# Performance work log

Measured on AMD Instinct MI355X. Metric: run time of the kernel, lower is better.

The kernel has to match this reference:

```python
import jax, jax.numpy as jnp
import numpy as np

B, S, F = 256, 512, 26
H, M, C = 512, 256, 20  # rnn_hidden, mlp_hidden, num_classes


def setup_inputs() -> dict:
    key = jax.random.key(0)
    ks = jax.random.split(key, 9)
    s_ih = 1.0 / np.sqrt(H)
    return {
        "x": jax.random.normal(ks[0], (B, S, F), dtype=jnp.float32),
        "w_ih": jax.random.uniform(ks[1], (4 * H, F), jnp.float32, -s_ih, s_ih),
        "w_hh": jax.random.uniform(ks[2], (4 * H, H), jnp.float32, -s_ih, s_ih),
        "b_ih": jax.random.uniform(ks[3], (4 * H,), jnp.float32, -s_ih, s_ih),
        "b_hh": jax.random.uniform(ks[4], (4 * H,), jnp.float32, -s_ih, s_ih),
        "w1": jax.random.uniform(ks[5], (M, H), jnp.float32, -s_ih, s_ih),
        "b1": jax.random.uniform(ks[6], (M,), jnp.float32, -s_ih, s_ih),
        "w2": jax.random.uniform(ks[7], (C, M), jnp.float32, -1.0 / np.sqrt(M), 1.0 / np.sqrt(M)),
        "b2": jax.random.uniform(ks[8], (C,), jnp.float32, -1.0 / np.sqrt(M), 1.0 / np.sqrt(M)),
    }


def reference(x, w_ih, w_hh, b_ih, b_hh, w1, b1, w2, b2):
    b, s, _ = x.shape
    h0 = jnp.zeros((b, H), x.dtype)
    c0 = jnp.zeros((b, H), x.dtype)
    bias = b_ih + b_hh

    def step(carry, xt):
        h, c = carry
        # original stores hx.data -> state carried into next step is detached
        h = jax.lax.stop_gradient(h)
        c = jax.lax.stop_gradient(c)
        z = xt @ w_ih.T + h @ w_hh.T + bias  # [b, 4H]
        i, f, g, o = jnp.split(z, 4, axis=-1)  # PyTorch gate order i,f,g,o
        c2 = jax.nn.sigmoid(f) * c + jax.nn.sigmoid(i) * jnp.tanh(g)
        h2 = jax.nn.sigmoid(o) * jnp.tanh(c2)
        return (h2, c2), h2

    _, hs = jax.lax.scan(step, (h0, c0), jnp.transpose(x, (1, 0, 2)))  # hs: [s, b, H]
    hs = jnp.transpose(hs, (1, 0, 2))  # [b, s, H]
    hidden = jax.nn.relu(jnp.einsum("bsh,mh->bsm", hs, w1) + b1)
    logits = jnp.einsum("bsm,cm->bsc", hidden, w2) + b2
    return jax.nn.log_softmax(logits, axis=-1)
```

## Files before the change

kernel.cpp:

```cpp
#include <hip/hip_runtime.h>

#define S_LEN 512
#define HID   512
#define FEAT  26
#define NCLS  20
#define DRING 16

typedef short bf16x8 __attribute__((ext_vector_type(8)));
typedef float f32x4  __attribute__((ext_vector_type(4)));

__device__ __forceinline__ unsigned short f2bf(float f) {
    unsigned u = __builtin_bit_cast(unsigned, f);
    unsigned r = (u + 0x7FFFu + ((u >> 16) & 1u)) >> 16;
    return (unsigned short)r;
}
__device__ __forceinline__ float sigm(float x) { return 1.f / (1.f + __expf(-x)); }
__device__ __forceinline__ float tanh_f(float x) {
    float xc = fminf(fmaxf(x, -15.f), 15.f);
    float t = __expf(-2.f * xc);
    return (1.f - t) / (1.f + t);
}

__device__ __forceinline__ void load4_coherent(const unsigned short* p,
                                               uint4& a0, uint4& a1, uint4& a2, uint4& a3) {
    asm volatile(
        "global_load_dwordx4 %0, %4, off sc0 sc1\n\t"
        "global_load_dwordx4 %1, %5, off sc0 sc1\n\t"
        "global_load_dwordx4 %2, %6, off sc0 sc1\n\t"
        "global_load_dwordx4 %3, %7, off sc0 sc1\n\t"
        "s_waitcnt vmcnt(0)"
        : "=&v"(a0), "=&v"(a1), "=&v"(a2), "=&v"(a3)
        : "v"(p), "v"(p + 8), "v"(p + 16), "v"(p + 24)
        : "memory");
}
__device__ __forceinline__ void store_coherent(unsigned short* p, unsigned d) {
    asm volatile(
        "global_store_dword %0, %1, off sc0 sc1\n\t"
        "s_waitcnt vmcnt(0)"
        :: "v"(p), "v"(d) : "memory");
}
__device__ __forceinline__ void store_coherent_x2(unsigned short* p, unsigned long long d) {
    asm volatile(
        "global_store_dwordx2 %0, %1, off sc0 sc1\n\t"
        "s_waitcnt vmcnt(0)"
        :: "v"(p), "v"(d) : "memory");
}
__device__ __forceinline__ void store_u32_nowait(unsigned* p, unsigned d) {
    asm volatile("global_store_dword %0, %1, off sc0 sc1" :: "v"(p), "v"(d) : "memory");
}
__device__ __forceinline__ unsigned load_u32_coherent(const unsigned* p) {
    unsigned v;
    asm volatile("global_load_dword %0, %1, off sc0 sc1\n\ts_waitcnt vmcnt(0)"
                 : "=v"(v) : "v"(p) : "memory");
    return v;
}
__device__ __forceinline__ void store_u32_sys_wait(unsigned* p, unsigned d) {
    asm volatile("global_store_dword %0, %1, off sc0 sc1\n\ts_waitcnt vmcnt(0)"
                 :: "v"(p), "v"(d) : "memory");
}

__device__ __forceinline__ void load4_l2(const unsigned short* p,
                                         uint4& a0, uint4& a1, uint4& a2, uint4& a3) {
    asm volatile(
        "global_load_dwordx4 %0, %4, off sc0\n\t"
        "global_load_dwordx4 %1, %5, off sc0\n\t"
        "global_load_dwordx4 %2, %6, off sc0\n\t"
        "global_load_dwordx4 %3, %7, off sc0\n\t"
        "s_waitcnt vmcnt(0)"
        : "=&v"(a0), "=&v"(a1), "=&v"(a2), "=&v"(a3)
        : "v"(p), "v"(p + 8), "v"(p + 16), "v"(p + 24)
        : "memory");
}
__device__ __forceinline__ void store_l2_x2(unsigned short* p, unsigned long long d) {
    asm volatile(
        "global_store_dwordx2 %0, %1, off sc0\n\t"
        "s_waitcnt vmcnt(0)"
        :: "v"(p), "v"(d) : "memory");
}
__device__ __forceinline__ void store_u32_nowait_l2(unsigned* p, unsigned d) {
    asm volatile("global_store_dword %0, %1, off sc0" :: "v"(p), "v"(d) : "memory");
}
__device__ __forceinline__ unsigned load_u32_l2(const unsigned* p) {
    unsigned v;
    asm volatile("global_load_dword %0, %1, off sc0\n\ts_waitcnt vmcnt(0)"
                 : "=v"(v) : "v"(p) : "memory");
    return v;
}

__global__ void prep_kernel(const float* __restrict__ w1, const float* __restrict__ w2,
                            unsigned short* __restrict__ w1b, unsigned short* __restrict__ w2b,
                            unsigned* __restrict__ syncw, int nclear) {
    int i = blockIdx.x * 256 + threadIdx.x;
    if (i < nclear) syncw[i] = 0u;
    if (i < 256 * 512) w1b[i] = f2bf(w1[i]);
    if (i < NCLS * 256) w2b[i] = f2bf(w2[i]);
}

__global__ __launch_bounds__(256, 1) void lstm_big_kernel(
    const float* __restrict__ x,
    const float* __restrict__ w_ih,
    const float* __restrict__ w_hh,
    const float* __restrict__ b_ih,
    const float* __restrict__ b_hh,
    const unsigned short* __restrict__ w1b,
    const float* __restrict__ b1,
    const unsigned short* __restrict__ w2b,
    const float* __restrict__ b2,
    float* __restrict__ out,
    unsigned short* __restrict__ hs,
    unsigned* __restrict__ flags)
{
    const int tid  = threadIdx.x;
    const int wave = tid >> 6;
    const int lane = tid & 63;
    const int quad = lane >> 4;
    const int l16  = lane & 15;

    const int  bx      = blockIdx.x;
    const int  xasm    = bx & 7;
    const int  kslt    = bx >> 3;
    const bool is_lstm = (kslt < 16);
    const int  ksub    = is_lstm ? kslt : (kslt - 16);
    const int  clust   = xasm * 2 + (ksub >> 3);
    const int  sub     = ksub & 7;

    __shared__ __align__(16) unsigned short At[16 * 552];
    __shared__ __align__(16) unsigned short hid[16 * 264];
    __shared__ float lg[16 * 24];
    __shared__ unsigned rdy;
    __shared__ unsigned fastf;
    if (tid == 0) rdy = 0u;

    {
        unsigned xcc;
        asm volatile("s_getreg_b32 %0, hwreg(HW_REG_XCC_ID)" : "=s"(xcc));
        if (tid == 0) {
            unsigned* slot = flags + (clust * 8 + sub) * 16 + (is_lstm ? 8 : 9);
            store_u32_sys_wait(slot, (xcc & 0xFu) + 1u);
        }
        if (wave == 0) {
            const unsigned* ps = flags + (clust * 8 + (lane & 7)) * 16 + ((lane & 8) ? 9 : 8);
            unsigned myx = 1u;
            for (;;) {
                unsigned v = 1u;
                if (lane < 16) v = load_u32_coherent(ps);
                if (__ballot(v != 0u) == ~0ull) { myx = v; break; }
                __builtin_amdgcn_s_sleep(2);
            }
            unsigned ref = __shfl(myx, 0);
            bool eq = (lane >= 16) || (myx == ref);
            if (tid == 0) fastf = (__ballot(eq) == ~0ull) ? 1u : 0u;
        }
    }
    __syncthreads();
    const bool fast = (fastf != 0u);

    if (is_lstm) {
        const int wic = sub;
        const int B0  = clust * 16;
        const int U0  = wic * 64;

        bf16x8 bB[4][17];
#pragma unroll
        for (int g = 0; g < 4; ++g) {
            const int row = g * 512 + U0 + wave * 16 + l16;
            const float* wrow = w_hh + (size_t)row * HID;
#pragma unroll
            for (int kk = 0; kk < 16; ++kk) {
                const float* p = wrow + kk * 32 + quad * 8;
                bf16x8 v;
#pragma unroll
                for (int j = 0; j < 8; ++j) v[j] = (short)f2bf(p[j]);
                bB[g][kk] = v;
            }
            const float* irow = w_ih + (size_t)row * FEAT;
            bf16x8 v;
#pragma unroll
            for (int j = 0; j < 8; ++j) {
                int ftr = quad * 8 + j;
                v[j] = (ftr < FEAT) ? (short)f2bf(irow[ftr]) : (short)0;
            }
            bB[g][16] = v;
        }

        float bias[4][4];
#pragma unroll
        for (int g = 0; g < 4; ++g)
#pragma unroll
            for (int r = 0; r < 4; ++r) {
                int rr = g * 512 + U0 + wave * 16 + quad * 4 + r;
                bias[g][r] = b_ih[rr] + b_hh[rr];
            }
        float cst[4] = {0.f, 0.f, 0.f, 0.f};

        const int sm = tid >> 4;
        const int sc = tid & 15;
        unsigned short* hsc = hs + (size_t)clust * S_LEN * 16 * HID;
        unsigned* myflag = flags + (clust * 8 + wic) * 16;
        const unsigned* peer = flags + (clust * 8 + (lane & 7)) * 16;

        for (int t = 0; t < S_LEN; ++t) {
            {
                unsigned pk = 0u;
                if (sc <= 12) {
                    float2 xv = *(const float2*)(x + ((size_t)(B0 + sm) * S_LEN + t) * FEAT + sc * 2);
                    pk = (unsigned)f2bf(xv.x) | ((unsigned)f2bf(xv.y) << 16);
                }
                *(unsigned*)(At + sm * 552 + 512 + sc * 2) = pk;
            }
            if (t > 0) {
                const unsigned tt = (unsigned)t;
                for (;;) {
                    unsigned v = ~0u;
                    if (lane < 8) v = fast ? load_u32_l2(peer) : load_u32_coherent(peer);
                    if (__ballot(v >= tt) == ~0ull) break;
                    if (!fast) __builtin_amdgcn_s_sleep(1);
                }
                const unsigned short* src =
                    hsc + ((size_t)(t - 1) * 16 + sm) * HID + sc * 32;
                unsigned short* dst = At + sm * 552 + sc * 32;
                uint4 a0, a1, a2, a3;
                if (fast) load4_l2(src, a0, a1, a2, a3);
                else      load4_coherent(src, a0, a1, a2, a3);
                *(uint4*)(dst)      = a0;
                *(uint4*)(dst + 8)  = a1;
                *(uint4*)(dst + 16) = a2;
                *(uint4*)(dst + 24) = a3;
            }
            __syncthreads();

            f32x4 acc[4];
#pragma unroll
            for (int g = 0; g < 4; ++g) acc[g] = (f32x4){0.f, 0.f, 0.f, 0.f};
            const unsigned short* arow = At + l16 * 552 + quad * 8;
            if (t > 0) {
#pragma unroll
                for (int kk = 0; kk < 17; ++kk) {
                    bf16x8 h = __builtin_bit_cast(bf16x8, *(const uint4*)(arow + kk * 32));
#pragma unroll
                    for (int g = 0; g < 4; ++g)
                        acc[g] = __builtin_amdgcn_mfma_f32_16x16x32_bf16(bB[g][kk], h, acc[g], 0, 0, 0);
                }
            } else {
                bf16x8 h = __builtin_bit_cast(bf16x8, *(const uint4*)(arow + 16 * 32));
#pragma unroll
                for (int g = 0; g < 4; ++g)
                    acc[g] = __builtin_amdgcn_mfma_f32_16x16x32_bf16(bB[g][16], h, acc[g], 0, 0, 0);
            }

            {
                unsigned short hv[4];
#pragma unroll
                for (int r = 0; r < 4; ++r) {
                    float zi = acc[0][r] + bias[0][r];
                    float zf = acc[1][r] + bias[1][r];
                    float zg = acc[2][r] + bias[2][r];
                    float zo = acc[3][r] + bias[3][r];
                    float cn = sigm(zf) * cst[r] + sigm(zi) * tanh_f(zg);
                    cst[r] = cn;
                    hv[r] = f2bf(sigm(zo) * tanh_f(cn));
                }
                unsigned long long d = (unsigned long long)hv[0]
                                     | ((unsigned long long)hv[1] << 16)
                                     | ((unsigned long long)hv[2] << 32)
                                     | ((unsigned long long)hv[3] << 48);
                unsigned short* hp = hsc + ((size_t)t * 16 + l16) * HID
                                   + U0 + wave * 16 + quad * 4;
                if (fast) store_l2_x2(hp, d);
                else      store_coherent_x2(hp, d);
            }
            __syncthreads();
            if (tid == 0) {
                if (fast) store_u32_nowait_l2(myflag, (unsigned)(t + 1));
                else      store_u32_nowait(myflag, (unsigned)(t + 1));
            }
        }
    } else {
        const int mc  = clust;
        const int m   = sub;
        const int B0  = mc * 16;
        const unsigned* peer = flags + (mc * 8 + (lane & 7)) * 16;
        const unsigned short* hsc = hs + (size_t)mc * S_LEN * 16 * HID;
        const int sm = tid >> 4;
        const int sc = tid & 15;

        for (int t = m; t < S_LEN; t += 8) {
            if (wave == 0) {
                for (;;) {
                    unsigned v = fast ? load_u32_l2(peer) : load_u32_coherent(peer);
                    if (__ballot(v >= (unsigned)(t + 1)) == ~0ull) break;
                    __builtin_amdgcn_s_sleep(8);
                }
                if (lane == 0)
                    __hip_atomic_store(&rdy, (unsigned)(t + 1), __ATOMIC_RELAXED,
                                       __HIP_MEMORY_SCOPE_WORKGROUP);
            } else {
                while (__hip_atomic_load(&rdy, __ATOMIC_RELAXED,
                                         __HIP_MEMORY_SCOPE_WORKGROUP) < (unsigned)(t + 1))
                    __builtin_amdgcn_s_sleep(8);
            }
            {
                const unsigned short* src = hsc + ((size_t)t * 16 + sm) * HID + sc * 32;
                unsigned short* dst = At + sm * 552 + sc * 32;
                uint4 a0, a1, a2, a3;
                if (fast) load4_l2(src, a0, a1, a2, a3);
                else      load4_coherent(src, a0, a1, a2, a3);
                *(uint4*)(dst)      = a0;
                *(uint4*)(dst + 8)  = a1;
                *(uint4*)(dst + 16) = a2;
                *(uint4*)(dst + 24) = a3;
            }
            __syncthreads();

            f32x4 a1[4];
#pragma unroll
            for (int nt = 0; nt < 4; ++nt) a1[nt] = (f32x4){0.f, 0.f, 0.f, 0.f};
#pragma unroll
            for (int kk = 0; kk < 16; ++kk) {
                bf16x8 a = __builtin_bit_cast(
                    bf16x8, *(const uint4*)(At + l16 * 552 + kk * 32 + quad * 8));
#pragma unroll
                for (int nt = 0; nt < 4; ++nt) {
                    int n = wave * 64 + nt * 16 + l16;
                    bf16x8 b = __builtin_bit_cast(
                        bf16x8, *(const uint4*)(w1b + (size_t)n * 512 + kk * 32 + quad * 8));
                    a1[nt] = __builtin_amdgcn_mfma_f32_16x16x32_bf16(a, b, a1[nt], 0, 0, 0);
                }
            }
#pragma unroll
            for (int nt = 0; nt < 4; ++nt) {
                int n = wave * 64 + nt * 16 + l16;
                float bv = b1[n];
#pragma unroll
                for (int r = 0; r < 4; ++r)
                    hid[(quad * 4 + r) * 264 + n] = f2bf(fmaxf(a1[nt][r] + bv, 0.f));
            }
            __syncthreads();
            if (wave == 0) {
                f32x4 a2[2];
                a2[0] = (f32x4){0.f, 0.f, 0.f, 0.f};
                a2[1] = (f32x4){0.f, 0.f, 0.f, 0.f};
#pragma unroll
                for (int kk = 0; kk < 8; ++kk) {
                    bf16x8 a = __builtin_bit_cast(
                        bf16x8, *(const uint4*)(hid + l16 * 264 + kk * 32 + quad * 8));
#pragma unroll
                    for (int nt = 0; nt < 2; ++nt) {
                        int n = nt * 16 + l16;
                        bf16x8 b;
                        if (n < NCLS) {
                            b = __builtin_bit_cast(
                                bf16x8, *(const uint4*)(w2b + (size_t)n * 256 + kk * 32 + quad * 8));
                        } else {
                            uint4 z; z.x = z.y = z.z = z.w = 0u;
                            b = __builtin_bit_cast(bf16x8, z);
                        }
                        a2[nt] = __builtin_amdgcn_mfma_f32_16x16x32_bf16(a, b, a2[nt], 0, 0, 0);
                    }
                }
#pragma unroll
                for (int nt = 0; nt < 2; ++nt) {
                    int n = nt * 16 + l16;
                    if (n < NCLS) {
                        float bv = b2[n];
#pragma unroll
                        for (int r = 0; r < 4; ++r)
                            lg[(quad * 4 + r) * 24 + n] = a2[nt][r] + bv;
                    }
                }
            }
            __syncthreads();
            if (tid < 16) {
                float v[NCLS];
                float mx = -3.4e38f;
#pragma unroll
                for (int c = 0; c < NCLS; ++c) { v[c] = lg[tid * 24 + c]; mx = fmaxf(mx, v[c]); }
                float s = 0.f;
#pragma unroll
                for (int c = 0; c < NCLS; ++c) s += __expf(v[c] - mx);
                float lse = mx + __logf(s);
                float* orow = out + ((size_t)(B0 + tid) * S_LEN + t) * NCLS;
#pragma unroll
                for (int c = 0; c < NCLS; ++c) orow[c] = v[c] - lse;
            }
            __syncthreads();
        }
    }
}

__global__ __launch_bounds__(256, 2) void lstm_fused_kernel(
    const float* __restrict__ x, const float* __restrict__ w_ih,
    const float* __restrict__ w_hh, const float* __restrict__ b_ih,
    const float* __restrict__ b_hh, const unsigned short* __restrict__ w1b,
    const float* __restrict__ b1, const unsigned short* __restrict__ w2b,
    const float* __restrict__ b2, float* __restrict__ out,
    unsigned short* __restrict__ hb, unsigned* __restrict__ flags,
    unsigned* __restrict__ done)
{
    const int tid  = threadIdx.x;
    const int wave = tid >> 6;
    const int lane = tid & 63;
    const int quad = lane >> 4;
    const int l16  = lane & 15;
    const int wg   = blockIdx.x;

    __shared__ __align__(16) unsigned short At[16 * 552];
    __shared__ float zb[16 * 132];
    __shared__ __align__(16) unsigned short hid[16 * 264];
    __shared__ float lg[16 * 24];
    __shared__ unsigned rdy;
    if (tid == 0) rdy = 0u;
    __syncthreads();

    if (wg < 256) {
        const int clust = (wg & 7) * 2 + (wg >= 128 ? 1 : 0);
        const int wic   = (wg >> 3) & 15;
        const int B0    = clust * 16;
        const int U0    = wic * 32;

        bf16x8 bB[2][17];
#pragma unroll
        for (int tl = 0; tl < 2; ++tl) {
            const int row = wave * 512 + U0 + tl * 16 + l16;
            const float* wrow = w_hh + (size_t)row * HID;
#pragma unroll
            for (int kk = 0; kk < 16; ++kk) {
                const float* p = wrow + kk * 32 + quad * 8;
                bf16x8 v;
#pragma unroll
                for (int j = 0; j < 8; ++j) v[j] = (short)f2bf(p[j]);
                bB[tl][kk] = v;
            }
            const float* irow = w_ih + (size_t)row * FEAT;
            bf16x8 v;
#pragma unroll
            for (int j = 0; j < 8; ++j) {
                int ftr = quad * 8 + j;
                v[j] = (ftr < FEAT) ? (short)f2bf(irow[ftr]) : (short)0;
            }
            bB[tl][16] = v;
        }

        const int gb = tid >> 4;
        const int gu = tid & 15;
        float bias[2][4];
#pragma unroll
        for (int uu = 0; uu < 2; ++uu)
#pragma unroll
            for (int g = 0; g < 4; ++g) {
                int r = g * 512 + U0 + 2 * gu + uu;
                bias[uu][g] = b_ih[r] + b_hh[r];
            }
        float cst[2] = {0.f, 0.f};

        const int sm = tid >> 4;
        const int sc = tid & 15;
        unsigned short* hbc = hb + (size_t)clust * DRING * 16 * HID;
        unsigned* myflag = flags + (clust * 16 + wic) * 16;
        const unsigned* peer = flags + (clust * 16 + (lane & 15)) * 16;

        for (int t = 0; t < S_LEN; ++t) {
            {
                unsigned pk = 0u;
                if (sc <= 12) {
                    float2 xv = *(const float2*)(x + ((size_t)(B0 + sm) * S_LEN + t) * FEAT + sc * 2);
                    pk = (unsigned)f2bf(xv.x) | ((unsigned)f2bf(xv.y) << 16);
                }
                *(unsigned*)(At + sm * 552 + 512 + sc * 2) = pk;
            }
            if (t > 0) {
                if (wave == 0) {
                    if (t >= DRING && lane == 0) {
                        const unsigned* dn = done + (clust * 8 + (t & 7)) * 16;
                        while (load_u32_coherent(dn) < (unsigned)(t - (DRING - 1)))
                            __builtin_amdgcn_s_sleep(8);
                    }
                    for (;;) {
                        unsigned v = load_u32_coherent(peer);
                        if (__ballot(v >= (unsigned)t) == ~0ull) break;
                        __builtin_amdgcn_s_sleep(1);
                    }
                    if (lane == 0)
                        __hip_atomic_store(&rdy, (unsigned)t, __ATOMIC_RELAXED,
                                           __HIP_MEMORY_SCOPE_WORKGROUP);
                } else {
                    while (__hip_atomic_load(&rdy, __ATOMIC_RELAXED,
                                             __HIP_MEMORY_SCOPE_WORKGROUP) < (unsigned)t)
                        __builtin_amdgcn_s_sleep(1);
                }
                const unsigned short* src =
                    hbc + ((t - 1) & (DRING - 1)) * 16 * HID + sm * HID + sc * 32;
                unsigned short* dst = At + sm * 552 + sc * 32;
                uint4 a0, a1, a2, a3;
                load4_coherent(src, a0, a1, a2, a3);
                *(uint4*)(dst)      = a0;
                *(uint4*)(dst + 8)  = a1;
                *(uint4*)(dst + 16) = a2;
                *(uint4*)(dst + 24) = a3;
            }
            __syncthreads();

            f32x4 acc0 = {0.f, 0.f, 0.f, 0.f};
            f32x4 acc1 = {0.f, 0.f, 0.f, 0.f};
            const unsigned short* arow = At + l16 * 552 + quad * 8;
            if (t > 0) {
#pragma unroll
                for (int kk = 0; kk < 17; ++kk) {
                    bf16x8 a = __builtin_bit_cast(bf16x8, *(const uint4*)(arow + kk * 32));
                    acc0 = __builtin_amdgcn_mfma_f32_16x16x32_bf16(a, bB[0][kk], acc0, 0, 0, 0);
                    acc1 = __builtin_amdgcn_mfma_f32_16x16x32_bf16(a, bB[1][kk], acc1, 0, 0, 0);
                }
            } else {
                bf16x8 a = __builtin_bit_cast(bf16x8, *(const uint4*)(arow + 16 * 32));
                acc0 = __builtin_amdgcn_mfma_f32_16x16x32_bf16(a, bB[0][16], acc0, 0, 0, 0);
                acc1 = __builtin_amdgcn_mfma_f32_16x16x32_bf16(a, bB[1][16], acc1, 0, 0, 0);
            }
#pragma unroll
            for (int r = 0; r < 4; ++r) {
                zb[(quad * 4 + r) * 132 + wave * 32 + l16]      = acc0[r];
                zb[(quad * 4 + r) * 132 + wave * 32 + 16 + l16] = acc1[r];
            }
            __syncthreads();

            {
                const float* zrow = zb + gb * 132;
                unsigned short hv2[2];
#pragma unroll
                for (int uu = 0; uu < 2; ++uu) {
                    int u = 2 * gu + uu;
                    float zi = zrow[u]      + bias[uu][0];
                    float zf = zrow[32 + u] + bias[uu][1];
                    float zg = zrow[64 + u] + bias[uu][2];
                    float zo = zrow[96 + u] + bias[uu][3];
                    float cn = sigm(zf) * cst[uu] + sigm(zi) * tanh_f(zg);
                    cst[uu] = cn;
                    hv2[uu] = f2bf(sigm(zo) * tanh_f(cn));
                }
                unsigned short* hp =
                    hbc + (t & (DRING - 1)) * 16 * HID + gb * HID + U0 + 2 * gu;
                store_coherent(hp, (unsigned)hv2[0] | ((unsigned)hv2[1] << 16));
            }
            __syncthreads();
            if (tid == 0) store_u32_nowait(myflag, (unsigned)(t + 1));
        }
    } else {
        const int mwg  = wg - 256;
        const int mc   = mwg >> 3;
        const int m    = mwg & 7;
        const int B0   = mc * 16;
        unsigned* mydone = done + (mc * 8 + m) * 16;
        const unsigned* peer = flags + (mc * 16 + (lane & 15)) * 16;
        const unsigned short* hbc = hb + (size_t)mc * DRING * 16 * HID;
        const int sm = tid >> 4;
        const int sc = tid & 15;

        for (int t = m; t < S_LEN; t += 8) {
            if (wave == 0) {
                for (;;) {
                    unsigned v = load_u32_coherent(peer);
                    if (__ballot(v >= (unsigned)(t + 1)) == ~0ull) break;
                    __builtin_amdgcn_s_sleep(8);
                }
                if (lane == 0)
                    __hip_atomic_store(&rdy, (unsigned)(t + 1), __ATOMIC_RELAXED,
                                       __HIP_MEMORY_SCOPE_WORKGROUP);
            } else {
                while (__hip_atomic_load(&rdy, __ATOMIC_RELAXED,
                                         __HIP_MEMORY_SCOPE_WORKGROUP) < (unsigned)(t + 1))
                    __builtin_amdgcn_s_sleep(8);
            }
            {
                const unsigned short* src =
                    hbc + (t & (DRING - 1)) * 16 * HID + sm * HID + sc * 32;
                unsigned short* dst = At + sm * 552 + sc * 32;
                uint4 a0, a1, a2, a3;
                load4_coherent(src, a0, a1, a2, a3);
                *(uint4*)(dst)      = a0;
                *(uint4*)(dst + 8)  = a1;
                *(uint4*)(dst + 16) = a2;
                *(uint4*)(dst + 24) = a3;
            }
            __syncthreads();
            if (tid == 0) store_u32_nowait(mydone, (unsigned)(t + 1));

            f32x4 a1[4];
#pragma unroll
            for (int nt = 0; nt < 4; ++nt) a1[nt] = (f32x4){0.f, 0.f, 0.f, 0.f};
#pragma unroll
            for (int kk = 0; kk < 16; ++kk) {
                bf16x8 a = __builtin_bit_cast(
                    bf16x8, *(const uint4*)(At + l16 * 552 + kk * 32 + quad * 8));
#pragma unroll
                for (int nt = 0; nt < 4; ++nt) {
                    int n = wave * 64 + nt * 16 + l16;
                    bf16x8 b = __builtin_bit_cast(
                        bf16x8, *(const uint4*)(w1b + (size_t)n * 512 + kk * 32 + quad * 8));
                    a1[nt] = __builtin_amdgcn_mfma_f32_16x16x32_bf16(a, b, a1[nt], 0, 0, 0);
                }
            }
#pragma unroll
            for (int nt = 0; nt < 4; ++nt) {
                int n = wave * 64 + nt * 16 + l16;
                float bv = b1[n];
#pragma unroll
                for (int r = 0; r < 4; ++r)
                    hid[(quad * 4 + r) * 264 + n] = f2bf(fmaxf(a1[nt][r] + bv, 0.f));
            }
            __syncthreads();
            if (wave == 0) {
                f32x4 a2[2];
                a2[0] = (f32x4){0.f, 0.f, 0.f, 0.f};
                a2[1] = (f32x4){0.f, 0.f, 0.f, 0.f};
#pragma unroll
                for (int kk = 0; kk < 8; ++kk) {
                    bf16x8 a = __builtin_bit_cast(
                        bf16x8, *(const uint4*)(hid + l16 * 264 + kk * 32 + quad * 8));
#pragma unroll
                    for (int nt = 0; nt < 2; ++nt) {
                        int n = nt * 16 + l16;
                        bf16x8 b;
                        if (n < NCLS) {
                            b = __builtin_bit_cast(
                                bf16x8, *(const uint4*)(w2b + (size_t)n * 256 + kk * 32 + quad * 8));
                        } else {
                            uint4 z; z.x = z.y = z.z = z.w = 0u;
                            b = __builtin_bit_cast(bf16x8, z);
                        }
                        a2[nt] = __builtin_amdgcn_mfma_f32_16x16x32_bf16(a, b, a2[nt], 0, 0, 0);
                    }
                }
#pragma unroll
                for (int nt = 0; nt < 2; ++nt) {
                    int n = nt * 16 + l16;
                    if (n < NCLS) {
                        float bv = b2[n];
#pragma unroll
                        for (int r = 0; r < 4; ++r)
                            lg[(quad * 4 + r) * 24 + n] = a2[nt][r] + bv;
                    }
                }
            }
            __syncthreads();
            if (tid < 16) {
                float v[NCLS];
                float mx = -3.4e38f;
#pragma unroll
                for (int c = 0; c < NCLS; ++c) { v[c] = lg[tid * 24 + c]; mx = fmaxf(mx, v[c]); }
                float s = 0.f;
#pragma unroll
                for (int c = 0; c < NCLS; ++c) s += __expf(v[c] - mx);
                float lse = mx + __logf(s);
                float* orow = out + ((size_t)(B0 + tid) * S_LEN + t) * NCLS;
#pragma unroll
                for (int c = 0; c < NCLS; ++c) orow[c] = v[c] - lse;
            }
            __syncthreads();
        }
    }
}

extern "C" void kernel_launch(void* const* d_in, const int* in_sizes, int n_in,
                              void* d_out, int out_size, void* d_ws, size_t ws_size,
                              hipStream_t stream) {
    const float* x    = (const float*)d_in[0];
    const float* w_ih = (const float*)d_in[1];
    const float* w_hh = (const float*)d_in[2];
    const float* b_ih = (const float*)d_in[3];
    const float* b_hh = (const float*)d_in[4];
    const float* w1   = (const float*)d_in[5];
    const float* b1   = (const float*)d_in[6];
    const float* w2   = (const float*)d_in[7];
    const float* b2   = (const float*)d_in[8];
    char* ws = (char*)d_ws;

    const size_t HS_BYTES = (size_t)16 * S_LEN * 16 * HID * 2;
    const size_t NEED_BIG = HS_BYTES + 8192 + 262144 + 10240;

    if (ws_size >= NEED_BIG) {
        unsigned short* hsb   = (unsigned short*)ws;
        unsigned*       flags = (unsigned*)(ws + HS_BYTES);
        unsigned short* w1b   = (unsigned short*)(ws + HS_BYTES + 8192);
        unsigned short* w2b   = (unsigned short*)(ws + HS_BYTES + 8192 + 262144);
        prep_kernel<<<512, 256, 0, stream>>>(w1, w2, w1b, w2b, flags, 2048);
        lstm_big_kernel<<<256, 256, 0, stream>>>(x, w_ih, w_hh, b_ih, b_hh,
                                                 w1b, b1, w2b, b2,
                                                 (float*)d_out, hsb, flags);
    } else {
        unsigned short* hb    = (unsigned short*)ws;
        unsigned*       flags = (unsigned*)(ws + 4194304);
        unsigned*       done  = (unsigned*)(ws + 4194304 + 16384);
        unsigned short* w1b   = (unsigned short*)(ws + 4194304 + 16384 + 8192);
        unsigned short* w2b   = (unsigned short*)(ws + 4194304 + 16384 + 8192 + 262144);
        prep_kernel<<<512, 256, 0, stream>>>(w1, w2, w1b, w2b, flags, 6144);
        lstm_fused_kernel<<<384, 256, 0, stream>>>(x, w_ih, w_hh, b_ih, b_hh,
                                                   w1b, b1, w2b, b2,
                                                   (float*)d_out, hb, flags, done);
    }
}
```

Measured before the change: 2.091 ms.

## Load h and x directly into MFMA registers, skipping LDS staging and barrier

Each wave now loads its MFMA B-operand fragments of the previous hidden state straight from global/L2 into registers, and builds the x fragment in registers, instead of staging through an LDS tile with a __syncthreads. Loads are issued without waiting and split with vmcnt(8), so the first half of the MFMAs overlaps the second half of the loads. This removes the LDS round trip and the block barrier from the serial recurrence critical path. In exchange each wave redundantly fetches the full h row set, which raises L2 traffic and register pressure.

```diff
diff --git a/kernel.cpp b/kernel.cpp
--- a/kernel.cpp
+++ b/kernel.cpp
@@ -58,6 +58,17 @@
     asm volatile("global_store_dword %0, %1, off sc0 sc1\n\ts_waitcnt vmcnt(0)"
                  :: "v"(p), "v"(d) : "memory");
 }
+__device__ __forceinline__ void load4_nw_sys(const unsigned short* p,
+                                             uint4& a0, uint4& a1, uint4& a2, uint4& a3) {
+    asm volatile(
+        "global_load_dwordx4 %0, %4, off sc0 sc1\n\t"
+        "global_load_dwordx4 %1, %5, off sc0 sc1\n\t"
+        "global_load_dwordx4 %2, %6, off sc0 sc1\n\t"
+        "global_load_dwordx4 %3, %7, off sc0 sc1"
+        : "=&v"(a0), "=&v"(a1), "=&v"(a2), "=&v"(a3)
+        : "v"(p), "v"(p + 32), "v"(p + 64), "v"(p + 96)
+        : "memory");
+}
 
 __device__ __forceinline__ void load4_l2(const unsigned short* p,
                                          uint4& a0, uint4& a1, uint4& a2, uint4& a3) {
@@ -85,6 +96,17 @@
     asm volatile("global_load_dword %0, %1, off sc0\n\ts_waitcnt vmcnt(0)"
                  : "=v"(v) : "v"(p) : "memory");
     return v;
+}
+__device__ __forceinline__ void load4_nw_l2(const unsigned short* p,
+                                            uint4& a0, uint4& a1, uint4& a2, uint4& a3) {
+    asm volatile(
+        "global_load_dwordx4 %0, %4, off sc0\n\t"
+        "global_load_dwordx4 %1, %5, off sc0\n\t"
+        "global_load_dwordx4 %2, %6, off sc0\n\t"
+        "global_load_dwordx4 %3, %7, off sc0"
+        : "=&v"(a0), "=&v"(a1), "=&v"(a2), "=&v"(a3)
+        : "v"(p), "v"(p + 32), "v"(p + 64), "v"(p + 96)
+        : "memory");
 }
 
 __global__ void prep_kernel(const float* __restrict__ w1, const float* __restrict__ w2,
@@ -193,21 +215,36 @@
             }
         float cst[4] = {0.f, 0.f, 0.f, 0.f};
 
-        const int sm = tid >> 4;
-        const int sc = tid & 15;
         unsigned short* hsc = hs + (size_t)clust * S_LEN * 16 * HID;
         unsigned* myflag = flags + (clust * 8 + wic) * 16;
         const unsigned* peer = flags + (clust * 8 + (lane & 7)) * 16;
+        const float* xrow = x + (size_t)(B0 + l16) * S_LEN * FEAT;
 
         for (int t = 0; t < S_LEN; ++t) {
+            bf16x8 xf;
             {
-                unsigned pk = 0u;
-                if (sc <= 12) {
-                    float2 xv = *(const float2*)(x + ((size_t)(B0 + sm) * S_LEN + t) * FEAT + sc * 2);
-                    pk = (unsigned)f2bf(xv.x) | ((unsigned)f2bf(xv.y) << 16);
-                }
-                *(unsigned*)(At + sm * 552 + 512 + sc * 2) = pk;
-            }
+                const float* xp = xrow + (size_t)t * FEAT + quad * 8;
+                float xv[8];
+                if (quad < 3) {
+                    float2 p0 = *(const float2*)(xp);
+                    float2 p1 = *(const float2*)(xp + 2);
+                    float2 p2 = *(const float2*)(xp + 4);
+                    float2 p3 = *(const float2*)(xp + 6);
+                    xv[0] = p0.x; xv[1] = p0.y; xv[2] = p1.x; xv[3] = p1.y;
+                    xv[4] = p2.x; xv[5] = p2.y; xv[6] = p3.x; xv[7] = p3.y;
+                } else {
+                    float2 p0 = *(const float2*)(xp);
+                    xv[0] = p0.x; xv[1] = p0.y;
+                    xv[2] = xv[3] = xv[4] = xv[5] = xv[6] = xv[7] = 0.f;
+                }
+#pragma unroll
+                for (int j = 0; j < 8; ++j) xf[j] = (short)f2bf(xv[j]);
+            }
+
+            f32x4 acc[4];
+#pragma unroll
+            for (int g = 0; g < 4; ++g) acc[g] = (f32x4){0.f, 0.f, 0.f, 0.f};
+
             if (t > 0) {
                 const unsigned tt = (unsigned)t;
                 for (;;) {
@@ -216,36 +253,52 @@
                     if (__ballot(v >= tt) == ~0ull) break;
                     if (!fast) __builtin_amdgcn_s_sleep(1);
                 }
-                const unsigned short* src =
-                    hsc + ((size_t)(t - 1) * 16 + sm) * HID + sc * 32;
-                unsigned short* dst = At + sm * 552 + sc * 32;
-                uint4 a0, a1, a2, a3;
-                if (fast) load4_l2(src, a0, a1, a2, a3);
-                else      load4_coherent(src, a0, a1, a2, a3);
-                *(uint4*)(dst)      = a0;
-                *(uint4*)(dst + 8)  = a1;
-                *(uint4*)(dst + 16) = a2;
-                *(uint4*)(dst + 24) = a3;
-            }
-            __syncthreads();
-
-            f32x4 acc[4];
-#pragma unroll
-            for (int g = 0; g < 4; ++g) acc[g] = (f32x4){0.f, 0.f, 0.f, 0.f};
-            const unsigned short* arow = At + l16 * 552 + quad * 8;
-            if (t > 0) {
-#pragma unroll
-                for (int kk = 0; kk < 17; ++kk) {
-                    bf16x8 h = __builtin_bit_cast(bf16x8, *(const uint4*)(arow + kk * 32));
-#pragma unroll
-                    for (int g = 0; g < 4; ++g)
-                        acc[g] = __builtin_amdgcn_mfma_f32_16x16x32_bf16(bB[g][kk], h, acc[g], 0, 0, 0);
+                const unsigned short* hrow =
+                    hsc + ((size_t)(t - 1) * 16 + l16) * HID + quad * 8;
+                uint4 hb0, hb1, hb2, hb3, hb4, hb5, hb6, hb7;
+                uint4 hb8, hb9, hb10, hb11, hb12, hb13, hb14, hb15;
+                if (fast) {
+                    load4_nw_l2(hrow,        hb0,  hb1,  hb2,  hb3);
+                    load4_nw_l2(hrow + 128,  hb4,  hb5,  hb6,  hb7);
+                    load4_nw_l2(hrow + 256,  hb8,  hb9,  hb10, hb11);
+                    load4_nw_l2(hrow + 384,  hb12, hb13, hb14, hb15);
+                } else {
+                    load4_nw_sys(hrow,       hb0,  hb1,  hb2,  hb3);
+                    load4_nw_sys(hrow + 128, hb4,  hb5,  hb6,  hb7);
+                    load4_nw_sys(hrow + 256, hb8,  hb9,  hb10, hb11);
+                    load4_nw_sys(hrow + 384, hb12, hb13, hb14, hb15);
+                }
+                asm volatile("s_waitcnt vmcnt(8)" ::: "memory");
+                __builtin_amdgcn_sched_barrier(0);
+#pragma unroll
+                for (int g = 0; g < 4; ++g) {
+                    acc[g] = __builtin_amdgcn_mfma_f32_16x16x32_bf16(bB[g][0], __builtin_bit_cast(bf16x8, hb0), acc[g], 0, 0, 0);
+                    acc[g] = __builtin_amdgcn_mfma_f32_16x16x32_bf16(bB[g][1], __builtin_bit_cast(bf16x8, hb1), acc[g], 0, 0, 0);
+                    acc[g] = __builtin_amdgcn_mfma_f32_16x16x32_bf16(bB[g][2], __builtin_bit_cast(bf16x8, hb2), acc[g], 0, 0, 0);
+                    acc[g] = __builtin_amdgcn_mfma_f32_16x16x32_bf16(bB[g][3], __builtin_bit_cast(bf16x8, hb3), acc[g], 0, 0, 0);
+                    acc[g] = __builtin_amdgcn_mfma_f32_16x16x32_bf16(bB[g][4], __builtin_bit_cast(bf16x8, hb4), acc[g], 0, 0, 0);
+                    acc[g] = __builtin_amdgcn_mfma_f32_16x16x32_bf16(bB[g][5], __builtin_bit_cast(bf16x8, hb5), acc[g], 0, 0, 0);
+                    acc[g] = __builtin_amdgcn_mfma_f32_16x16x32_bf16(bB[g][6], __builtin_bit_cast(bf16x8, hb6), acc[g], 0, 0, 0);
+                    acc[g] = __builtin_amdgcn_mfma_f32_16x16x32_bf16(bB[g][7], __builtin_bit_cast(bf16x8, hb7), acc[g], 0, 0, 0);
+                }
+                asm volatile("s_waitcnt vmcnt(0)" ::: "memory");
+                __builtin_amdgcn_sched_barrier(0);
+#pragma unroll
+                for (int g = 0; g < 4; ++g) {
+                    acc[g] = __builtin_amdgcn_mfma_f32_16x16x32_bf16(bB[g][8],  __builtin_bit_cast(bf16x8, hb8),  acc[g], 0, 0, 0);
+                    acc[g] = __builtin_amdgcn_mfma_f32_16x16x32_bf16(bB[g][9],  __builtin_bit_cast(bf16x8, hb9),  acc[g], 0, 0, 0);
+                    acc[g] = __builtin_amdgcn_mfma_f32_16x16x32_bf16(bB[g][10], __builtin_bit_cast(bf16x8, hb10), acc[g], 0, 0, 0);
+                    acc[g] = __builtin_amdgcn_mfma_f32_16x16x32_bf16(bB[g][11], __builtin_bit_cast(bf16x8, hb11), acc[g], 0, 0, 0);
+                    acc[g] = __builtin_amdgcn_mfma_f32_16x16x32_bf16(bB[g][12], __builtin_bit_cast(bf16x8, hb12), acc[g], 0, 0, 0);
+                    acc[g] = __builtin_amdgcn_mfma_f32_16x16x32_bf16(bB[g][13], __builtin_bit_cast(bf16x8, hb13), acc[g], 0, 0, 0);
+                    acc[g] = __builtin_amdgcn_mfma_f32_16x16x32_bf16(bB[g][14], __builtin_bit_cast(bf16x8, hb14), acc[g], 0, 0, 0);
+                    acc[g] = __builtin_amdgcn_mfma_f32_16x16x32_bf16(bB[g][15], __builtin_bit_cast(bf16x8, hb15), acc[g], 0, 0, 0);
+                    acc[g] = __builtin_amdgcn_mfma_f32_16x16x32_bf16(bB[g][16], xf, acc[g], 0, 0, 0);
                 }
             } else {
-                bf16x8 h = __builtin_bit_cast(bf16x8, *(const uint4*)(arow + 16 * 32));
 #pragma unroll
                 for (int g = 0; g < 4; ++g)
-                    acc[g] = __builtin_amdgcn_mfma_f32_16x16x32_bf16(bB[g][16], h, acc[g], 0, 0, 0);
+                    acc[g] = __builtin_amdgcn_mfma_f32_16x16x32_bf16(bB[g][16], xf, acc[g], 0, 0, 0);
             }
 
             {
```

Measured after the change: 2.477 ms. 18.5% more time.

## Split recurrent h exchange into halves, overlapping second-half load with MFMA

Applied to the files above, without the earlier changes.

The per-step wait on peer flags is split: a workgroup first waits only for the four producers of the first half of h, loads that half, and issues the x-projection and first eight K-slices of MFMAs while the second half is being fetched. A second barrier then publishes the second half before the remaining MFMAs run. Bias is folded into the accumulator initialisation, removing the per-element adds. This aims to hide global-memory latency of the inter-workgroup h exchange behind compute. In exchange it adds an extra workgroup barrier per step and relies on hand-placed waitcnt and sched_barrier ordering being correct.

```diff
diff --git a/kernel.cpp b/kernel.cpp
--- a/kernel.cpp
+++ b/kernel.cpp
@@ -58,6 +58,12 @@
     asm volatile("global_store_dword %0, %1, off sc0 sc1\n\ts_waitcnt vmcnt(0)"
                  :: "v"(p), "v"(d) : "memory");
 }
+__device__ __forceinline__ void load2_nw_sys(const unsigned short* p, uint4& a0, uint4& a1) {
+    asm volatile(
+        "global_load_dwordx4 %0, %2, off sc0 sc1\n\t"
+        "global_load_dwordx4 %1, %3, off sc0 sc1"
+        : "=&v"(a0), "=&v"(a1) : "v"(p), "v"(p + 8) : "memory");
+}
 
 __device__ __forceinline__ void load4_l2(const unsigned short* p,
                                          uint4& a0, uint4& a1, uint4& a2, uint4& a3) {
@@ -85,6 +91,12 @@
     asm volatile("global_load_dword %0, %1, off sc0\n\ts_waitcnt vmcnt(0)"
                  : "=v"(v) : "v"(p) : "memory");
     return v;
+}
+__device__ __forceinline__ void load2_nw_l2(const unsigned short* p, uint4& a0, uint4& a1) {
+    asm volatile(
+        "global_load_dwordx4 %0, %2, off sc0\n\t"
+        "global_load_dwordx4 %1, %3, off sc0"
+        : "=&v"(a0), "=&v"(a1) : "v"(p), "v"(p + 8) : "memory");
 }
 
 __global__ void prep_kernel(const float* __restrict__ w1, const float* __restrict__ w2,
@@ -183,13 +195,13 @@
             bB[g][16] = v;
         }
 
-        float bias[4][4];
+        f32x4 biasv[4];
 #pragma unroll
         for (int g = 0; g < 4; ++g)
 #pragma unroll
             for (int r = 0; r < 4; ++r) {
                 int rr = g * 512 + U0 + wave * 16 + quad * 4 + r;
-                bias[g][r] = b_ih[rr] + b_hh[rr];
+                biasv[g][r] = b_ih[rr] + b_hh[rr];
             }
         float cst[4] = {0.f, 0.f, 0.f, 0.f};
 
@@ -208,57 +220,101 @@
                 }
                 *(unsigned*)(At + sm * 552 + 512 + sc * 2) = pk;
             }
+
+            f32x4 acc[4];
+#pragma unroll
+            for (int g = 0; g < 4; ++g) acc[g] = biasv[g];
+
             if (t > 0) {
                 const unsigned tt = (unsigned)t;
+                unsigned long long bal;
                 for (;;) {
                     unsigned v = ~0u;
                     if (lane < 8) v = fast ? load_u32_l2(peer) : load_u32_coherent(peer);
-                    if (__ballot(v >= tt) == ~0ull) break;
+                    bal = __ballot(v >= tt);
+                    if ((bal & 0xFull) == 0xFull) break;
                     if (!fast) __builtin_amdgcn_s_sleep(1);
                 }
-                const unsigned short* src =
-                    hsc + ((size_t)(t - 1) * 16 + sm) * HID + sc * 32;
-                unsigned short* dst = At + sm * 552 + sc * 32;
-                uint4 a0, a1, a2, a3;
-                if (fast) load4_l2(src, a0, a1, a2, a3);
-                else      load4_coherent(src, a0, a1, a2, a3);
-                *(uint4*)(dst)      = a0;
-                *(uint4*)(dst + 8)  = a1;
-                *(uint4*)(dst + 16) = a2;
-                *(uint4*)(dst + 24) = a3;
-            }
-            __syncthreads();
-
-            f32x4 acc[4];
-#pragma unroll
-            for (int g = 0; g < 4; ++g) acc[g] = (f32x4){0.f, 0.f, 0.f, 0.f};
-            const unsigned short* arow = At + l16 * 552 + quad * 8;
-            if (t > 0) {
-#pragma unroll
-                for (int kk = 0; kk < 17; ++kk) {
+                const bool g1ok = ((bal >> 4) & 0xFull) == 0xFull;
+
+                const unsigned short* srow = hsc + ((size_t)(t - 1) * 16 + sm) * HID;
+                uint4 s0, s1, s2, s3;
+                if (fast) load2_nw_l2(srow + sc * 16, s0, s1);
+                else      load2_nw_sys(srow + sc * 16, s0, s1);
+
+                if (!g1ok) {
+                    for (;;) {
+                        unsigned v = ~0u;
+                        if (lane >= 4 && lane < 8)
+                            v = fast ? load_u32_l2(peer) : load_u32_coherent(peer);
+                        unsigned long long b2_ = __ballot(v >= tt);
+                        if (((b2_ >> 4) & 0xFull) == 0xFull) break;
+                        if (!fast) __builtin_amdgcn_s_sleep(1);
+                    }
+                }
+                asm volatile("s_waitcnt vmcnt(0)" ::: "memory");
+                __builtin_amdgcn_sched_barrier(0);
+                {
+                    unsigned short* dst = At + sm * 552 + sc * 16;
+                    *(uint4*)(dst)     = s0;
+                    *(uint4*)(dst + 8) = s1;
+                }
+                if (fast) load2_nw_l2(srow + 256 + sc * 16, s2, s3);
+                else      load2_nw_sys(srow + 256 + sc * 16, s2, s3);
+
+                asm volatile("s_waitcnt lgkmcnt(0)" ::: "memory");
+                __builtin_amdgcn_sched_barrier(0);
+                __builtin_amdgcn_s_barrier();
+
+                const unsigned short* arow = At + l16 * 552 + quad * 8;
+                {
+                    bf16x8 hx = __builtin_bit_cast(bf16x8, *(const uint4*)(arow + 16 * 32));
+#pragma unroll
+                    for (int g = 0; g < 4; ++g)
+                        acc[g] = __builtin_amdgcn_mfma_f32_16x16x32_bf16(bB[g][16], hx, acc[g], 0, 0, 0);
+                }
+#pragma unroll
+                for (int kk = 0; kk < 8; ++kk) {
                     bf16x8 h = __builtin_bit_cast(bf16x8, *(const uint4*)(arow + kk * 32));
 #pragma unroll
                     for (int g = 0; g < 4; ++g)
                         acc[g] = __builtin_amdgcn_mfma_f32_16x16x32_bf16(bB[g][kk], h, acc[g], 0, 0, 0);
                 }
+
+                asm volatile("s_waitcnt vmcnt(0)" ::: "memory");
+                __builtin_amdgcn_sched_barrier(0);
+                {
+                    unsigned short* dst = At + sm * 552 + 256 + sc * 16;
+                    *(uint4*)(dst)     = s2;
+                    *(uint4*)(dst + 8) = s3;
+                }
+                asm volatile("s_waitcnt lgkmcnt(0)" ::: "memory");
+                __builtin_amdgcn_sched_barrier(0);
+                __builtin_amdgcn_s_barrier();
+
+#pragma unroll
+                for (int kk = 8; kk < 16; ++kk) {
+                    bf16x8 h = __builtin_bit_cast(bf16x8, *(const uint4*)(arow + kk * 32));
+#pragma unroll
+                    for (int g = 0; g < 4; ++g)
+                        acc[g] = __builtin_amdgcn_mfma_f32_16x16x32_bf16(bB[g][kk], h, acc[g], 0, 0, 0);
+                }
             } else {
-                bf16x8 h = __builtin_bit_cast(bf16x8, *(const uint4*)(arow + 16 * 32));
+                __syncthreads();
+                const unsigned short* arow = At + l16 * 552 + quad * 8;
+                bf16x8 hx = __builtin_bit_cast(bf16x8, *(const uint4*)(arow + 16 * 32));
 #pragma unroll
                 for (int g = 0; g < 4; ++g)
-                    acc[g] = __builtin_amdgcn_mfma_f32_16x16x32_bf16(bB[g][16], h, acc[g], 0, 0, 0);
+                    acc[g] = __builtin_amdgcn_mfma_f32_16x16x32_bf16(bB[g][16], hx, acc[g], 0, 0, 0);
             }
 
             {
                 unsigned short hv[4];
 #pragma unroll
                 for (int r = 0; r < 4; ++r) {
-                    float zi = acc[0][r] + bias[0][r];
-                    float zf = acc[1][r] + bias[1][r];
-                    float zg = acc[2][r] + bias[2][r];
-                    float zo = acc[3][r] + bias[3][r];
-                    float cn = sigm(zf) * cst[r] + sigm(zi) * tanh_f(zg);
+                    float cn = sigm(acc[1][r]) * cst[r] + sigm(acc[0][r]) * tanh_f(acc[2][r]);
                     cst[r] = cn;
-                    hv[r] = f2bf(sigm(zo) * tanh_f(cn));
+                    hv[r] = f2bf(sigm(acc[3][r]) * tanh_f(cn));
                 }
                 unsigned long long d = (unsigned long long)hv[0]
                                      | ((unsigned long long)hv[1] << 16)
```

Result: faster. 1.946 ms (-6.9%).
